# Performance work log

Measured on AMD Instinct MI355X. Metric: run time of the kernel, lower is better.

Reference implementation:

```python
import jax, jax.numpy as jnp
import numpy as np

B, NUM_ATOMS, NUM_CHANNELS, MAX_L = 4, 4096, 32, 3


def setup_inputs() -> dict:
    key = jax.random.key(0)
    ks = jax.random.split(key, MAX_L + 1)
    inp = {}
    for l in range(MAX_L + 1):
        # parts[l]: [b, num_atoms, 1, 2l+1, num_channels]
        inp[f"part{l}"] = jax.random.normal(
            ks[l], (B, NUM_ATOMS, 1, 2 * l + 1, NUM_CHANNELS), dtype=jnp.float32
        )
    return inp


def reference(part0, part1, part2, part3):
    b, a = part0.shape[0], part0.shape[1]
    c = part0.shape[-1]
    # scalars_part0: reshape of l=0 part -> [b, atoms, C]
    scalars0 = part0.reshape(b, a, c)
    # SO(3)-invariant norm: per-l channel Gram matrix reduced over the m axis.
    # Ordering matches the torch loop: l-major, channel1-major, channel2-minor.
    grams = []
    for p in (part0, part1, part2, part3):
        g = jnp.einsum("banmc,banmd->bacd", p, p)  # [b, atoms, C, C]
        grams.append(g.reshape(b, a, c * c))
    return jnp.concatenate([scalars0] + grams, axis=-1)  # [b, atoms, C + (max_l+1)*C^2]
```

## Files before the change

### kernel.cpp

```cpp
#include <hip/hip_runtime.h>


constexpr int C = 32;
constexpr int OUT_PER_ATOM = C + 4 * C * C;
constexpr int ROWS = 16;
constexpr int NQ = OUT_PER_ATOM / 4;

__global__ __launch_bounds__(256) void getscalars_kernel(
    const float* __restrict__ p0, const float* __restrict__ p1,
    const float* __restrict__ p2, const float* __restrict__ p3,
    float* __restrict__ out)
{
    __shared__ float lds[ROWS * C];

    const int atom = blockIdx.x;
    const int t = threadIdx.x;

    const float* s0 = p0 + (size_t)atom * (1 * C);
    const float* s1 = p1 + (size_t)atom * (3 * C);
    const float* s2 = p2 + (size_t)atom * (5 * C);
    const float* s3 = p3 + (size_t)atom * (7 * C);

    for (int i = t; i < ROWS * C; i += 256) {
        const int row = i >> 5;
        const int col = i & 31;
        float v;
        if (row < 1)      v = s0[col];
        else if (row < 4) v = s1[(row - 1) * C + col];
        else if (row < 9) v = s2[(row - 4) * C + col];
        else              v = s3[(row - 9) * C + col];
        lds[i] = v;
    }
    __syncthreads();

    float4* o4 = reinterpret_cast<float4*>(out + (size_t)atom * OUT_PER_ATOM);

    for (int q = t; q < NQ; q += 256) {
        float4 r;
        if (q < C / 4) {
            r.x = lds[4 * q + 0];
            r.y = lds[4 * q + 1];
            r.z = lds[4 * q + 2];
            r.w = lds[4 * q + 3];
        } else {
            const int jj  = 4 * q - C;
            const int l   = jj >> 10;
            const int rem = jj & 1023;
            const int c   = rem >> 5;
            const int d   = rem & 31;
            const int row0 = l * l;
            const int nm   = 2 * l + 1;

            float a0 = 0.f, a1 = 0.f, a2 = 0.f, a3 = 0.f;
            for (int m = 0; m < nm; ++m) {
                const float* rowp = &lds[(row0 + m) * C];
                const float pc = rowp[c];
                a0 += pc * rowp[d + 0];
                a1 += pc * rowp[d + 1];
                a2 += pc * rowp[d + 2];
                a3 += pc * rowp[d + 3];
            }
            r.x = a0; r.y = a1; r.z = a2; r.w = a3;
        }
        o4[q] = r;
    }
}

extern "C" void kernel_launch(void* const* d_in, const int* in_sizes, int n_in,
                              void* d_out, int out_size, void* d_ws, size_t ws_size,
                              hipStream_t stream) {
    const float* p0 = (const float*)d_in[0];
    const float* p1 = (const float*)d_in[1];
    const float* p2 = (const float*)d_in[2];
    const float* p3 = (const float*)d_in[3];
    float* out = (float*)d_out;

    const int natoms = in_sizes[0] / C;
    getscalars_kernel<<<natoms, 256, 0, stream>>>(p0, p1, p2, p3, out);
}
```

Before: 68.81 us.

## Vectorize atom loads and give each thread fixed gram outputs across all l

The global-to-LDS load now uses one float4 per thread (128 threads) instead of a branchy scalar loop. Each thread owns one (c, d..d+3) output position and reads all 16 rows of c and d values from LDS into registers once. It then computes the four per-l Gram entries with fully unrolled code, which removes the per-output index arithmetic, the variable-trip m loops and the strided q loop. This raises register use per thread. The kernel is mostly bound by output writes, so the gain may be limited.

```diff
diff --git a/kernel.cpp b/kernel.cpp
--- a/kernel.cpp
+++ b/kernel.cpp
@@ -3,67 +3,75 @@
 
 constexpr int C = 32;
 constexpr int OUT_PER_ATOM = C + 4 * C * C;
-constexpr int ROWS = 16;
-constexpr int NQ = OUT_PER_ATOM / 4;
 
 __global__ __launch_bounds__(256) void getscalars_kernel(
     const float* __restrict__ p0, const float* __restrict__ p1,
     const float* __restrict__ p2, const float* __restrict__ p3,
     float* __restrict__ out)
 {
-    __shared__ float lds[ROWS * C];
+    __shared__ float lds[16 * C];
 
     const int atom = blockIdx.x;
     const int t = threadIdx.x;
 
-    const float* s0 = p0 + (size_t)atom * (1 * C);
-    const float* s1 = p1 + (size_t)atom * (3 * C);
-    const float* s2 = p2 + (size_t)atom * (5 * C);
-    const float* s3 = p3 + (size_t)atom * (7 * C);
-
-    for (int i = t; i < ROWS * C; i += 256) {
-        const int row = i >> 5;
-        const int col = i & 31;
-        float v;
-        if (row < 1)      v = s0[col];
-        else if (row < 4) v = s1[(row - 1) * C + col];
-        else if (row < 9) v = s2[(row - 4) * C + col];
-        else              v = s3[(row - 9) * C + col];
-        lds[i] = v;
+    if (t < 128) {
+        const float4* src;
+        int idx;
+        if (t < 8)       { src = (const float4*)(p0 + (size_t)atom * 32);  idx = t; }
+        else if (t < 32) { src = (const float4*)(p1 + (size_t)atom * 96);  idx = t - 8; }
+        else if (t < 72) { src = (const float4*)(p2 + (size_t)atom * 160); idx = t - 32; }
+        else             { src = (const float4*)(p3 + (size_t)atom * 224); idx = t - 72; }
+        reinterpret_cast<float4*>(lds)[t] = src[idx];
     }
     __syncthreads();
 
-    float4* o4 = reinterpret_cast<float4*>(out + (size_t)atom * OUT_PER_ATOM);
+    const int c = t >> 3;
+    const int d = (t & 7) * 4;
 
-    for (int q = t; q < NQ; q += 256) {
-        float4 r;
-        if (q < C / 4) {
-            r.x = lds[4 * q + 0];
-            r.y = lds[4 * q + 1];
-            r.z = lds[4 * q + 2];
-            r.w = lds[4 * q + 3];
-        } else {
-            const int jj  = 4 * q - C;
-            const int l   = jj >> 10;
-            const int rem = jj & 1023;
-            const int c   = rem >> 5;
-            const int d   = rem & 31;
-            const int row0 = l * l;
-            const int nm   = 2 * l + 1;
+    float  pc[16];
+    float4 pd[16];
+    #pragma unroll
+    for (int r = 0; r < 16; ++r) {
+        pc[r] = lds[r * C + c];
+        pd[r] = *reinterpret_cast<const float4*>(&lds[r * C + d]);
+    }
 
-            float a0 = 0.f, a1 = 0.f, a2 = 0.f, a3 = 0.f;
-            for (int m = 0; m < nm; ++m) {
-                const float* rowp = &lds[(row0 + m) * C];
-                const float pc = rowp[c];
-                a0 += pc * rowp[d + 0];
-                a1 += pc * rowp[d + 1];
-                a2 += pc * rowp[d + 2];
-                a3 += pc * rowp[d + 3];
-            }
-            r.x = a0; r.y = a1; r.z = a2; r.w = a3;
-        }
-        o4[q] = r;
+    float* outp = out + (size_t)atom * OUT_PER_ATOM;
+
+    if (t < 8) {
+        reinterpret_cast<float4*>(outp)[t] = reinterpret_cast<const float4*>(lds)[t];
     }
+
+    float4 g;
+    g.x = pc[0] * pd[0].x;
+    g.y = pc[0] * pd[0].y;
+    g.z = pc[0] * pd[0].z;
+    g.w = pc[0] * pd[0].w;
+    *reinterpret_cast<float4*>(outp + C + 0 * 1024 + 4 * t) = g;
+
+    g.x = pc[1] * pd[1].x; g.y = pc[1] * pd[1].y; g.z = pc[1] * pd[1].z; g.w = pc[1] * pd[1].w;
+    #pragma unroll
+    for (int r = 2; r <= 3; ++r) {
+        g.x += pc[r] * pd[r].x; g.y += pc[r] * pd[r].y;
+        g.z += pc[r] * pd[r].z; g.w += pc[r] * pd[r].w;
+    }
+    *reinterpret_cast<float4*>(outp + C + 1 * 1024 + 4 * t) = g;
+
+    g.x = pc[4] * pd[4].x; g.y = pc[4] * pd[4].y; g.z = pc[4] * pd[4].z; g.w = pc[4] * pd[4].w;
+    #pragma unroll
+    for (int r = 5; r <= 8; ++r) {
+        g.x += pc[r] * pd[r].x; g.y += pc[r] * pd[r].y;
+        g.z += pc[r] * pd[r].z; g.w += pc[r] * pd[r].w;
+    }
+    *reinterpret_cast<float4*>(outp + C + 2 * 1024 + 4 * t) = g;
+
+    g.x = pc[9] * pd[9].x; g.y = pc[9] * pd[9].y; g.z = pc[9] * pd[9].z; g.w = pc[9] * pd[9].w;
+    #pragma unroll
+    for (int r = 10; r <= 15; ++r) {
+        g.x += pc[r] * pd[r].x; g.y += pc[r] * pd[r].y;
+        g.z += pc[r] * pd[r].z; g.w += pc[r] * pd[r].w;
+    }
+    *reinterpret_cast<float4*>(outp + C + 3 * 1024 + 4 * t) = g;
 }
 
 extern "C" void kernel_launch(void* const* d_in, const int* in_sizes, int n_in,
```

Result: faster. 64.98 us (-5.6%).
